# Performance work log

Measured on AMD Instinct MI355X. Metric: run time of the kernel, lower is better.

## Reference

```python
import jax, jax.numpy as jnp
import numpy as np

B, NA, C, NG = 32, 32768, 81, 24
POS_IOU, NEG_IOU, NPR = 0.5, 0.4, 3
VXY, VWH = 0.1, 0.2
NEG_BIG = 1e30


def cxcywh_to_xyxy(b):
    xy, wh = b[..., :2], b[..., 2:]
    return jnp.concatenate([xy - 0.5 * wh, xy + 0.5 * wh], axis=-1)


def box_iou_xyxy(a, g):
    # a: [Na,4], g: [Ng,4] -> [Na,Ng]
    lt = jnp.maximum(a[:, None, :2], g[None, :, :2])
    rb = jnp.minimum(a[:, None, 2:], g[None, :, 2:])
    wh = jnp.clip(rb - lt, 0.0)
    inter = wh[..., 0] * wh[..., 1]
    area_a = (a[:, 2] - a[:, 0]) * (a[:, 3] - a[:, 1])
    area_g = (g[:, 2] - g[:, 0]) * (g[:, 3] - g[:, 1])
    union = area_a[:, None] + area_g[None, :] - inter
    return inter / jnp.maximum(union, 1e-12)


def encode_ssd(gt, anc):
    # gt, anc: [N,4] cxcywh
    txy = (gt[:, :2] - anc[:, :2]) / anc[:, 2:] / VXY
    twh = jnp.log(gt[:, 2:] / anc[:, 2:]) / VWH
    return jnp.concatenate([txy, twh], axis=-1)


def match_one(anchors, gt_b, gt_l):
    # anchors: [Na,4], gt_b: [Ng,4], gt_l: [Ng]
    iou = box_iou_xyxy(cxcywh_to_xyxy(anchors), cxcywh_to_xyxy(gt_b))  # [Na,Ng]
    iou_max = iou.max(axis=1)
    gt_idx = jnp.argmax(iou, axis=1)          # [Na]
    best_anchor = jnp.argmax(iou, axis=0)     # [Ng]
    pos = (iou_max >= POS_IOU).at[best_anchor].set(True)
    ign = (iou_max > NEG_IOU) & ~pos
    cls_t = jnp.where(pos, gt_l[gt_idx].astype(jnp.int32), jnp.where(ign, -1, 0))
    box_t = encode_ssd(gt_b[gt_idx], anchors) * pos[:, None].astype(jnp.float32)
    return cls_t, box_t, pos


def setup_inputs() -> dict:
    key = jax.random.key(0)
    k1, k2, k3, k4, k5, k6, k7 = jax.random.split(key, 7)
    cls_pred = jax.random.normal(k1, (B, NA, C), jnp.float32)
    box_pred = jax.random.normal(k2, (B, NA, 4), jnp.float32) * 0.5
    a_xy = jax.random.uniform(k3, (NA, 2), jnp.float32)
    a_wh = jax.random.uniform(k4, (NA, 2), jnp.float32, minval=0.02, maxval=0.5)
    anchors = jnp.concatenate([a_xy, a_wh], axis=-1)
    g_xy = jax.random.uniform(k5, (B, NG, 2), jnp.float32)
    g_wh = jax.random.uniform(k6, (B, NG, 2), jnp.float32, minval=0.05, maxval=0.4)
    gt_boxes = jnp.concatenate([g_xy, g_wh], axis=-1)
    gt_labels = jax.random.randint(k7, (B, NG), 1, C, jnp.int32)
    return {"cls_pred": cls_pred, "box_pred": box_pred, "anchors": anchors,
            "gt_boxes": gt_boxes, "gt_labels": gt_labels}


def reference(cls_pred, box_pred, anchors, gt_boxes, gt_labels):
    # matching is @torch.no_grad -> constants
    cls_t, box_t, pos = jax.vmap(lambda b, l: match_one(anchors, b, l))(gt_boxes, gt_labels)
    box_t = jax.lax.stop_gradient(box_t)

    logp = jax.nn.log_softmax(cls_pred, axis=-1)
    tgt = jnp.clip(cls_t, 0)
    ce = -jnp.take_along_axis(logp, tgt[..., None], axis=-1)[..., 0]  # [B,Na]

    posf = pos.astype(jnp.float32)
    num_pos = posf.sum(-1)                       # [B]
    pos_ce_sum = (ce * posf).sum(-1)
    neg_mask = cls_t == 0
    neg_count = neg_mask.sum(-1).astype(jnp.float32)

    # descending sort of negative CE (hard-negative mining)
    neg_sorted = -jnp.sort(-jnp.where(neg_mask, ce, -NEG_BIG), axis=-1)  # [B,Na]
    ranks = jnp.arange(NA, dtype=jnp.float32)[None, :]

    num_neg = jnp.minimum(NPR * num_pos, neg_count)
    topk_sum = (neg_sorted * (ranks < num_neg[:, None])).sum(-1)
    cls_pos = jnp.where(num_neg > 0,
                        (pos_ce_sum + topk_sum) / jnp.maximum(num_pos + num_neg, 1.0),
                        pos_ce_sum / jnp.maximum(num_pos, 1.0))

    num_neg0 = jnp.minimum(100.0, neg_count)
    topk0_sum = (neg_sorted * (ranks < num_neg0[:, None])).sum(-1)
    cls_zero = jnp.where(num_neg0 > 0, topk0_sum / jnp.maximum(num_neg0, 1.0), 0.0)

    cls_loss = jnp.where(num_pos > 0, cls_pos, cls_zero)

    d = box_pred - box_t
    ad = jnp.abs(d)
    sl1 = jnp.where(ad < 1.0, 0.5 * d * d, ad - 0.5)
    reg_sum = (sl1 * posf[..., None]).sum((-1, -2))
    reg = jnp.where(num_pos > 0, reg_sum / jnp.maximum(num_pos * 4.0, 1.0), 0.0)

    return cls_loss.mean(), reg.mean(), num_pos.sum() / B
```

## Files before the change

### kernel.cpp

```cpp
#include <hip/hip_runtime.h>
#include <math.h>

#define B_  32
#define NA_ 32768
#define C_  81
#define NG_ 24

typedef const __attribute__((address_space(1))) unsigned int* gas_ptr;
typedef __attribute__((address_space(3))) unsigned int* las_ptr;

__device__ inline float wave_max_f(float v) {
  #pragma unroll
  for (int s = 32; s >= 1; s >>= 1) v = fmaxf(v, __shfl_xor(v, s));
  return v;
}
__device__ inline float wave_sum_f(float v) {
  #pragma unroll
  for (int s = 32; s >= 1; s >>= 1) v += __shfl_xor(v, s);
  return v;
}

__global__ void k_init(unsigned long long* best_packed, int* num_pos_g, int* notneg_g,
                       float* pos_ce_g, float* reg_sum_g) {
  const int t = threadIdx.x + blockIdx.x * blockDim.x;
  if (t < B_ * NG_) best_packed[t] = 0ULL;
  if (t < B_) { num_pos_g[t] = 0; notneg_g[t] = 0; pos_ce_g[t] = 0.f; reg_sum_g[t] = 0.f; }
}

__global__ __launch_bounds__(256) void k_match(
    const float* __restrict__ anchors, const float* __restrict__ gt_boxes,
    float* __restrict__ iou_max_out, int* __restrict__ gt_idx_out,
    unsigned long long* __restrict__ best_packed)
{
  const int b = blockIdx.y;
  const int a = blockIdx.x * 256 + threadIdx.x;
  __shared__ float4 gt_sh[NG_];
  __shared__ float gt_area_sh[NG_];
  __shared__ unsigned long long best_sh[NG_];
  if (threadIdx.x < NG_) {
    const float* g = gt_boxes + ((size_t)b * NG_ + threadIdx.x) * 4;
    float cx = g[0], cy = g[1], w = g[2], h = g[3];
    float x0 = cx - 0.5f * w, y0 = cy - 0.5f * h, x1 = cx + 0.5f * w, y1 = cy + 0.5f * h;
    gt_sh[threadIdx.x] = make_float4(x0, y0, x1, y1);
    gt_area_sh[threadIdx.x] = (x1 - x0) * (y1 - y0);
    best_sh[threadIdx.x] = 0ULL;
  }
  __syncthreads();
  const float4 anc = ((const float4*)anchors)[a];
  const float ax0 = anc.x - 0.5f * anc.z, ay0 = anc.y - 0.5f * anc.w;
  const float ax1 = anc.x + 0.5f * anc.z, ay1 = anc.y + 0.5f * anc.w;
  const float area_a = (ax1 - ax0) * (ay1 - ay0);
  float best_iou = -1.0f; int best_g = 0;
  const int lane = threadIdx.x & 63;
  const int wave_base = a - lane;
  for (int g = 0; g < NG_; ++g) {
    const float4 G = gt_sh[g];
    float lx = fmaxf(ax0, G.x), ly = fmaxf(ay0, G.y);
    float rx = fminf(ax1, G.z), ry = fminf(ay1, G.w);
    float ww = fmaxf(rx - lx, 0.f), hh = fmaxf(ry - ly, 0.f);
    float inter = ww * hh;
    float uni = area_a + gt_area_sh[g] - inter;
    float iou = inter / fmaxf(uni, 1e-12f);
    if (iou > best_iou) { best_iou = iou; best_g = g; }
    const float m = wave_max_f(iou);
    const unsigned long long mk = __ballot(iou == m);
    if (lane == 0) {
      const int amin = wave_base + (__ffsll((long long)mk) - 1);
      const unsigned long long key =
          ((unsigned long long)__float_as_uint(m) << 32) | (unsigned)(~(unsigned)amin);
      atomicMax(&best_sh[g], key);
    }
  }
  const size_t idx = (size_t)b * NA_ + a;
  iou_max_out[idx] = best_iou;
  gt_idx_out[idx]  = best_g;
  __syncthreads();
  if (threadIdx.x < NG_)
    atomicMax(&best_packed[b * NG_ + threadIdx.x], best_sh[threadIdx.x]);
}

#define TPB 128
__global__ __launch_bounds__(128) void k_ce(
    const float* __restrict__ cls_pred, const float* __restrict__ box_pred,
    const float* __restrict__ anchors, const float* __restrict__ gt_boxes,
    const int* __restrict__ gt_labels,
    const float* __restrict__ iou_max_in, const int* __restrict__ gt_idx_in,
    const unsigned long long* __restrict__ best_packed,
    int* __restrict__ neg_bits,
    int* __restrict__ num_pos_g, int* __restrict__ notneg_g,
    float* __restrict__ pos_ce_g, float* __restrict__ reg_sum_g)
{
  __shared__ float tile[TPB * C_];
  __shared__ int best_a_sh[NG_];
  __shared__ int label_sh[NG_];
  __shared__ int np_sh[2], nn_sh[2];
  __shared__ float pce_sh[2], reg_sh[2];
  const int b = blockIdx.y;
  const int tid = threadIdx.x;
  const int wave = tid >> 6, lane = tid & 63;
  const int a0 = blockIdx.x * TPB;
  const int a = a0 + tid;
  const size_t idx = (size_t)b * NA_ + a;

  if (tid < NG_) {
    best_a_sh[tid] = (int)(~(unsigned)(best_packed[b * NG_ + tid]));
    label_sh[tid]  = gt_labels[b * NG_ + tid];
  }

  {
    const unsigned int* gtile =
        (const unsigned int*)(cls_pred + ((size_t)b * NA_ + a0) * C_);
    las_ptr lbase = (las_ptr)tile;
    #pragma unroll
    for (int k = 0; k < 20; ++k) {
      const int chunk = k * TPB + tid;
      const int wbase = k * TPB + wave * 64;
      __builtin_amdgcn_global_load_lds((gas_ptr)(gtile + (size_t)chunk * 4),
                                       lbase + (size_t)wbase * 4, 16, 0, 0);
    }
    if (tid < 32) {
      const int chunk = 20 * TPB + tid;
      __builtin_amdgcn_global_load_lds((gas_ptr)(gtile + (size_t)chunk * 4),
                                       lbase + (size_t)(20 * TPB) * 4, 16, 0, 0);
    }
  }

  const float imax = iou_max_in[idx];
  const int gi = gt_idx_in[idx];
  __syncthreads();

  bool pos = (imax >= 0.5f);
  #pragma unroll
  for (int g = 0; g < NG_; ++g) pos = pos || (best_a_sh[g] == a);
  const bool ign = (imax > 0.4f) && !pos;
  const bool neg = !pos && !ign;
  const int tgt = pos ? label_sh[gi] : 0;

  const float* row = &tile[tid * C_];
  float sum = 0.f;
  #pragma unroll 27
  for (int j = 0; j < C_; ++j) sum += __expf(row[j]);
  float ce = fmaxf(__logf(sum) - row[tgt], 0.f);

  neg_bits[idx] = neg ? __float_as_int(ce) : -1;

  float pce = 0.f, reg = 0.f;
  if (pos) {
    pce = ce;
    const float4 bp = ((const float4*)box_pred)[idx];
    const float4 an = ((const float4*)anchors)[a];
    const float* gt = gt_boxes + ((size_t)b * NG_ + gi) * 4;
    const float tx = (gt[0] - an.x) / an.z / 0.1f;
    const float ty = (gt[1] - an.y) / an.w / 0.1f;
    const float tw = logf(gt[2] / an.z) / 0.2f;
    const float th = logf(gt[3] / an.w) / 0.2f;
    float d, ad;
    d = bp.x - tx; ad = fabsf(d); reg += (ad < 1.f) ? 0.5f * d * d : (ad - 0.5f);
    d = bp.y - ty; ad = fabsf(d); reg += (ad < 1.f) ? 0.5f * d * d : (ad - 0.5f);
    d = bp.z - tw; ad = fabsf(d); reg += (ad < 1.f) ? 0.5f * d * d : (ad - 0.5f);
    d = bp.w - th; ad = fabsf(d); reg += (ad < 1.f) ? 0.5f * d * d : (ad - 0.5f);
  }

  const int np_w = __popcll(__ballot(pos));
  const int nn_w = __popcll(__ballot(pos || ign));
  const float pce_w = wave_sum_f(pce);
  const float reg_w = wave_sum_f(reg);
  if (lane == 0) { np_sh[wave] = np_w; nn_sh[wave] = nn_w; pce_sh[wave] = pce_w; reg_sh[wave] = reg_w; }
  __syncthreads();
  if (tid == 0) {
    const int np = np_sh[0] + np_sh[1];
    const int nn = nn_sh[0] + nn_sh[1];
    const float pc = pce_sh[0] + pce_sh[1];
    const float rg = reg_sh[0] + reg_sh[1];
    if (np) atomicAdd(&num_pos_g[b], np);
    if (nn) atomicAdd(&notneg_g[b], nn);
    if (pc != 0.f) atomicAdd(&pos_ce_g[b], pc);
    if (rg != 0.f) atomicAdd(&reg_sum_g[b], rg);
  }
}

__global__ __launch_bounds__(1024) void k_select(
    const int* __restrict__ neg_bits,
    const int* __restrict__ num_pos_g, const int* __restrict__ notneg_g,
    const float* __restrict__ pos_ce_g, const float* __restrict__ reg_sum_g,
    float* __restrict__ cls_out, float* __restrict__ reg_out)
{
  const int b = blockIdx.x;
  const int t = threadIdx.x;
  const int wave = t >> 6, lane = t & 63;
  int v[32];
  const int* src = neg_bits + (size_t)b * NA_;
  #pragma unroll
  for (int i = 0; i < 32; ++i) v[i] = src[t + (i << 10)];
  const int np = num_pos_g[b];
  const int negc = NA_ - notneg_g[b];
  const int k1 = min(3 * np, negc);
  const int k0 = min(100, negc);
  __shared__ unsigned red_sh[16];
  __shared__ unsigned bc_sh;
  int T1 = 0, T0 = 0;
  for (int bit = 30; bit >= 0; --bit) {
    const int t1 = T1 | (1 << bit);
    const int t0 = T0 | (1 << bit);
    unsigned c = 0;
    #pragma unroll
    for (int i = 0; i < 32; ++i) {
      if (v[i] >= t1) c += (1u << 16);
      if (v[i] >= t0) c += 1u;
    }
    #pragma unroll
    for (int s = 32; s >= 1; s >>= 1) c += __shfl_xor(c, s);
    if (lane == 0) red_sh[wave] = c;
    __syncthreads();
    if (t == 0) {
      unsigned sum = 0;
      for (int w = 0; w < 16; ++w) sum += red_sh[w];
      bc_sh = sum;
    }
    __syncthreads();
    const unsigned sum = bc_sh;
    if ((int)(sum >> 16) >= k1 && k1 > 0) T1 = t1;
    if ((int)(sum & 0xFFFFu) >= k0 && k0 > 0) T0 = t0;
    __syncthreads();
  }
  float s1 = 0.f, s0 = 0.f; unsigned cg = 0;
  #pragma unroll
  for (int i = 0; i < 32; ++i) {
    const int x = v[i];
    if (x > T1) { s1 += __int_as_float(x); cg += (1u << 16); }
    if (x > T0) { s0 += __int_as_float(x); cg += 1u; }
  }
  #pragma unroll
  for (int s = 32; s >= 1; s >>= 1) {
    s1 += __shfl_xor(s1, s); s0 += __shfl_xor(s0, s); cg += __shfl_xor(cg, s);
  }
  __shared__ float f1_sh[16], f0_sh[16]; __shared__ unsigned cg_sh[16];
  if (lane == 0) { f1_sh[wave] = s1; f0_sh[wave] = s0; cg_sh[wave] = cg; }
  __syncthreads();
  if (t == 0) {
    float S1 = 0.f, S0 = 0.f; unsigned CG = 0;
    for (int w = 0; w < 16; ++w) { S1 += f1_sh[w]; S0 += f0_sh[w]; CG += cg_sh[w]; }
    const int cg1 = (int)(CG >> 16), cg0 = (int)(CG & 0xFFFFu);
    const float topk1 = (k1 > 0) ? (S1 + (float)(k1 - cg1) * __int_as_float(T1)) : 0.f;
    const float topk0 = (k0 > 0) ? (S0 + (float)(k0 - cg0) * __int_as_float(T0)) : 0.f;
    const float npf = (float)np;
    const float pce = pos_ce_g[b];
    float cls;
    if (np > 0)
      cls = (k1 > 0) ? (pce + topk1) / fmaxf(npf + (float)k1, 1.f)
                     : pce / fmaxf(npf, 1.f);
    else
      cls = (k0 > 0) ? topk0 / fmaxf((float)k0, 1.f) : 0.f;
    cls_out[b] = cls;
    reg_out[b] = (np > 0) ? reg_sum_g[b] / fmaxf(npf * 4.f, 1.f) : 0.f;
  }
}

__global__ __launch_bounds__(64) void k_final(
    const float* __restrict__ cls_out, const float* __restrict__ reg_out,
    const int* __restrict__ num_pos_g, float* __restrict__ out)
{
  const int t = threadIdx.x;
  float c = (t < B_) ? cls_out[t] : 0.f;
  float r = (t < B_) ? reg_out[t] : 0.f;
  float n = (t < B_) ? (float)num_pos_g[t] : 0.f;
  #pragma unroll
  for (int s = 32; s >= 1; s >>= 1) {
    c += __shfl_xor(c, s); r += __shfl_xor(r, s); n += __shfl_xor(n, s);
  }
  if (t == 0) { out[0] = c / (float)B_; out[1] = r / (float)B_; out[2] = n / (float)B_; }
}

extern "C" void kernel_launch(void* const* d_in, const int* in_sizes, int n_in,
                              void* d_out, int out_size, void* d_ws, size_t ws_size,
                              hipStream_t stream) {
  const float* cls_pred  = (const float*)d_in[0];
  const float* box_pred  = (const float*)d_in[1];
  const float* anchors   = (const float*)d_in[2];
  const float* gt_boxes  = (const float*)d_in[3];
  const int*   gt_labels = (const int*)d_in[4];
  float* out = (float*)d_out;

  char* ws = (char*)d_ws;
  unsigned long long* best_packed = (unsigned long long*)ws;
  int*   num_pos_g = (int*)(ws + 6144);
  int*   notneg_g  = (int*)(ws + 6144 + 128);
  float* pos_ce_g  = (float*)(ws + 6144 + 256);
  float* reg_sum_g = (float*)(ws + 6144 + 384);
  float* cls_out   = (float*)(ws + 6144 + 512);
  float* reg_out   = (float*)(ws + 6144 + 640);
  float* iou_max   = (float*)(ws + 8192);
  int*   gt_idx    = (int*)(ws + 8192 + (size_t)4 * B_ * NA_);
  int*   neg_bits  = (int*)(ws + 8192 + (size_t)8 * B_ * NA_);

  hipLaunchKernelGGL(k_init, dim3(1), dim3(768), 0, stream,
                     best_packed, num_pos_g, notneg_g, pos_ce_g, reg_sum_g);
  hipLaunchKernelGGL(k_match, dim3(NA_ / 256, B_), dim3(256), 0, stream,
                     anchors, gt_boxes, iou_max, gt_idx, best_packed);
  hipLaunchKernelGGL(k_ce, dim3(NA_ / TPB, B_), dim3(TPB), 0, stream,
                     cls_pred, box_pred, anchors, gt_boxes, gt_labels,
                     iou_max, gt_idx, best_packed, neg_bits,
                     num_pos_g, notneg_g, pos_ce_g, reg_sum_g);
  hipLaunchKernelGGL(k_select, dim3(B_), dim3(1024), 0, stream,
                     neg_bits, num_pos_g, notneg_g, pos_ce_g, reg_sum_g, cls_out, reg_out);
  hipLaunchKernelGGL(k_final, dim3(1), dim3(64), 0, stream,
                     cls_out, reg_out, num_pos_g, out);
}
```

Measured before the change: 588.0 us.

## Split per-gt best-anchor search into separate kernel and drop init/final launches

Per-gt best-anchor argmax moves out of the per-anchor match kernel, which did a wave max, ballot and shared atomic every iteration. A new kernel gives each (gt, batch) pair one block that scans all anchors with a packed 64-bit key and reduces with shuffles. The init and final kernels are folded in: counters and the output are zeroed in the new kernel, and the select kernel atomically accumulates the batch means into the output. The select kernel also uses vectorized loads and per-bit shared atomic counters, removing two barriers per radix bit. This trades fewer launches and lighter match work for a redundant full anchor scan per gt (768 blocks) and non-deterministic float atomic ordering in the final output.

```diff
diff --git a/kernel.cpp b/kernel.cpp
--- a/kernel.cpp
+++ b/kernel.cpp
@@ -9,41 +9,31 @@
 typedef const __attribute__((address_space(1))) unsigned int* gas_ptr;
 typedef __attribute__((address_space(3))) unsigned int* las_ptr;
 
-__device__ inline float wave_max_f(float v) {
-  #pragma unroll
-  for (int s = 32; s >= 1; s >>= 1) v = fmaxf(v, __shfl_xor(v, s));
-  return v;
-}
 __device__ inline float wave_sum_f(float v) {
   #pragma unroll
   for (int s = 32; s >= 1; s >>= 1) v += __shfl_xor(v, s);
   return v;
 }
-
-__global__ void k_init(unsigned long long* best_packed, int* num_pos_g, int* notneg_g,
-                       float* pos_ce_g, float* reg_sum_g) {
-  const int t = threadIdx.x + blockIdx.x * blockDim.x;
-  if (t < B_ * NG_) best_packed[t] = 0ULL;
-  if (t < B_) { num_pos_g[t] = 0; notneg_g[t] = 0; pos_ce_g[t] = 0.f; reg_sum_g[t] = 0.f; }
-}
-
-__global__ __launch_bounds__(256) void k_match(
+__device__ inline unsigned long long shflx_u64(unsigned long long v, int s) {
+  int lo = __shfl_xor((int)(unsigned)(v & 0xFFFFFFFFULL), s);
+  int hi = __shfl_xor((int)(unsigned)(v >> 32), s);
+  return ((unsigned long long)(unsigned)hi << 32) | (unsigned)lo;
+}
+
+__global__ __launch_bounds__(256) void k_match_a(
     const float* __restrict__ anchors, const float* __restrict__ gt_boxes,
-    float* __restrict__ iou_max_out, int* __restrict__ gt_idx_out,
-    unsigned long long* __restrict__ best_packed)
+    float* __restrict__ iou_max_out, int* __restrict__ gt_idx_out)
 {
   const int b = blockIdx.y;
   const int a = blockIdx.x * 256 + threadIdx.x;
   __shared__ float4 gt_sh[NG_];
   __shared__ float gt_area_sh[NG_];
-  __shared__ unsigned long long best_sh[NG_];
   if (threadIdx.x < NG_) {
     const float* g = gt_boxes + ((size_t)b * NG_ + threadIdx.x) * 4;
     float cx = g[0], cy = g[1], w = g[2], h = g[3];
     float x0 = cx - 0.5f * w, y0 = cy - 0.5f * h, x1 = cx + 0.5f * w, y1 = cy + 0.5f * h;
     gt_sh[threadIdx.x] = make_float4(x0, y0, x1, y1);
     gt_area_sh[threadIdx.x] = (x1 - x0) * (y1 - y0);
-    best_sh[threadIdx.x] = 0ULL;
   }
   __syncthreads();
   const float4 anc = ((const float4*)anchors)[a];
@@ -51,8 +41,7 @@
   const float ax1 = anc.x + 0.5f * anc.z, ay1 = anc.y + 0.5f * anc.w;
   const float area_a = (ax1 - ax0) * (ay1 - ay0);
   float best_iou = -1.0f; int best_g = 0;
-  const int lane = threadIdx.x & 63;
-  const int wave_base = a - lane;
+  #pragma unroll 4
   for (int g = 0; g < NG_; ++g) {
     const float4 G = gt_sh[g];
     float lx = fmaxf(ax0, G.x), ly = fmaxf(ay0, G.y);
@@ -62,21 +51,57 @@
     float uni = area_a + gt_area_sh[g] - inter;
     float iou = inter / fmaxf(uni, 1e-12f);
     if (iou > best_iou) { best_iou = iou; best_g = g; }
-    const float m = wave_max_f(iou);
-    const unsigned long long mk = __ballot(iou == m);
-    if (lane == 0) {
-      const int amin = wave_base + (__ffsll((long long)mk) - 1);
-      const unsigned long long key =
-          ((unsigned long long)__float_as_uint(m) << 32) | (unsigned)(~(unsigned)amin);
-      atomicMax(&best_sh[g], key);
-    }
   }
   const size_t idx = (size_t)b * NA_ + a;
   iou_max_out[idx] = best_iou;
   gt_idx_out[idx]  = best_g;
-  __syncthreads();
-  if (threadIdx.x < NG_)
-    atomicMax(&best_packed[b * NG_ + threadIdx.x], best_sh[threadIdx.x]);
+}
+
+__global__ __launch_bounds__(256) void k_match_b(
+    const float* __restrict__ anchors, const float* __restrict__ gt_boxes,
+    int* __restrict__ best_anchor,
+    int* num_pos_g, int* notneg_g, float* pos_ce_g, float* reg_sum_g, float* out)
+{
+  const int g = blockIdx.x, b = blockIdx.y;
+  const int tid = threadIdx.x, wave = tid >> 6, lane = tid & 63;
+  if (g == 0 && b == 0) {
+    if (tid < B_) { num_pos_g[tid] = 0; notneg_g[tid] = 0; pos_ce_g[tid] = 0.f; reg_sum_g[tid] = 0.f; }
+    else if (tid < B_ + 3) out[tid - B_] = 0.f;
+  }
+  const float* gp = gt_boxes + ((size_t)b * NG_ + g) * 4;
+  const float gx0 = gp[0] - 0.5f * gp[2], gy0 = gp[1] - 0.5f * gp[3];
+  const float gx1 = gp[0] + 0.5f * gp[2], gy1 = gp[1] + 0.5f * gp[3];
+  const float area_g = (gx1 - gx0) * (gy1 - gy0);
+  unsigned long long key = 0ULL;
+  #pragma unroll 4
+  for (int i = 0; i < NA_ / 256; ++i) {
+    const int a = i * 256 + tid;
+    const float4 anc = ((const float4*)anchors)[a];
+    const float ax0 = anc.x - 0.5f * anc.z, ay0 = anc.y - 0.5f * anc.w;
+    const float ax1 = anc.x + 0.5f * anc.z, ay1 = anc.y + 0.5f * anc.w;
+    float lx = fmaxf(ax0, gx0), ly = fmaxf(ay0, gy0);
+    float rx = fminf(ax1, gx1), ry = fminf(ay1, gy1);
+    float ww = fmaxf(rx - lx, 0.f), hh = fmaxf(ry - ly, 0.f);
+    float inter = ww * hh;
+    float uni = (ax1 - ax0) * (ay1 - ay0) + area_g - inter;
+    float iou = inter / fmaxf(uni, 1e-12f);
+    unsigned long long k2 =
+        ((unsigned long long)__float_as_uint(iou) << 32) | (unsigned)(~(unsigned)a);
+    if (k2 > key) key = k2;
+  }
+  #pragma unroll
+  for (int s = 32; s >= 1; s >>= 1) {
+    unsigned long long o = shflx_u64(key, s);
+    if (o > key) key = o;
+  }
+  __shared__ unsigned long long red[4];
+  if (lane == 0) red[wave] = key;
+  __syncthreads();
+  if (tid == 0) {
+    unsigned long long k = red[0];
+    for (int w = 1; w < 4; ++w) if (red[w] > k) k = red[w];
+    best_anchor[b * NG_ + g] = (int)(~(unsigned)k);
+  }
 }
 
 #define TPB 128
@@ -85,7 +110,7 @@
     const float* __restrict__ anchors, const float* __restrict__ gt_boxes,
     const int* __restrict__ gt_labels,
     const float* __restrict__ iou_max_in, const int* __restrict__ gt_idx_in,
-    const unsigned long long* __restrict__ best_packed,
+    const int* __restrict__ best_anchor,
     int* __restrict__ neg_bits,
     int* __restrict__ num_pos_g, int* __restrict__ notneg_g,
     float* __restrict__ pos_ce_g, float* __restrict__ reg_sum_g)
@@ -103,7 +128,7 @@
   const size_t idx = (size_t)b * NA_ + a;
 
   if (tid < NG_) {
-    best_a_sh[tid] = (int)(~(unsigned)(best_packed[b * NG_ + tid]));
+    best_a_sh[tid] = best_anchor[b * NG_ + tid];
     label_sh[tid]  = gt_labels[b * NG_ + tid];
   }
 
@@ -183,21 +208,24 @@
     const int* __restrict__ neg_bits,
     const int* __restrict__ num_pos_g, const int* __restrict__ notneg_g,
     const float* __restrict__ pos_ce_g, const float* __restrict__ reg_sum_g,
-    float* __restrict__ cls_out, float* __restrict__ reg_out)
+    float* __restrict__ out)
 {
   const int b = blockIdx.x;
   const int t = threadIdx.x;
   const int wave = t >> 6, lane = t & 63;
+  __shared__ unsigned cnt_sh[32];
+  __shared__ float f1_sh[16], f0_sh[16];
+  __shared__ unsigned cg_sh[16];
+  if (t < 32) cnt_sh[t] = 0;
   int v[32];
-  const int* src = neg_bits + (size_t)b * NA_;
-  #pragma unroll
-  for (int i = 0; i < 32; ++i) v[i] = src[t + (i << 10)];
+  const int4* src4 = (const int4*)(neg_bits + (size_t)b * NA_);
+  #pragma unroll
+  for (int i = 0; i < 8; ++i) *(int4*)&v[4 * i] = src4[t + (i << 10)];
   const int np = num_pos_g[b];
   const int negc = NA_ - notneg_g[b];
   const int k1 = min(3 * np, negc);
   const int k0 = min(100, negc);
-  __shared__ unsigned red_sh[16];
-  __shared__ unsigned bc_sh;
+  __syncthreads();
   int T1 = 0, T0 = 0;
   for (int bit = 30; bit >= 0; --bit) {
     const int t1 = T1 | (1 << bit);
@@ -210,18 +238,11 @@
     }
     #pragma unroll
     for (int s = 32; s >= 1; s >>= 1) c += __shfl_xor(c, s);
-    if (lane == 0) red_sh[wave] = c;
+    if (lane == 0) atomicAdd(&cnt_sh[bit], c);
     __syncthreads();
-    if (t == 0) {
-      unsigned sum = 0;
-      for (int w = 0; w < 16; ++w) sum += red_sh[w];
-      bc_sh = sum;
-    }
-    __syncthreads();
-    const unsigned sum = bc_sh;
+    const unsigned sum = cnt_sh[bit];
     if ((int)(sum >> 16) >= k1 && k1 > 0) T1 = t1;
     if ((int)(sum & 0xFFFFu) >= k0 && k0 > 0) T0 = t0;
-    __syncthreads();
   }
   float s1 = 0.f, s0 = 0.f; unsigned cg = 0;
   #pragma unroll
@@ -234,7 +255,6 @@
   for (int s = 32; s >= 1; s >>= 1) {
     s1 += __shfl_xor(s1, s); s0 += __shfl_xor(s0, s); cg += __shfl_xor(cg, s);
   }
-  __shared__ float f1_sh[16], f0_sh[16]; __shared__ unsigned cg_sh[16];
   if (lane == 0) { f1_sh[wave] = s1; f0_sh[wave] = s0; cg_sh[wave] = cg; }
   __syncthreads();
   if (t == 0) {
@@ -251,24 +271,11 @@
                      : pce / fmaxf(npf, 1.f);
     else
       cls = (k0 > 0) ? topk0 / fmaxf((float)k0, 1.f) : 0.f;
-    cls_out[b] = cls;
-    reg_out[b] = (np > 0) ? reg_sum_g[b] / fmaxf(npf * 4.f, 1.f) : 0.f;
-  }
-}
-
-__global__ __launch_bounds__(64) void k_final(
-    const float* __restrict__ cls_out, const float* __restrict__ reg_out,
-    const int* __restrict__ num_pos_g, float* __restrict__ out)
-{
-  const int t = threadIdx.x;
-  float c = (t < B_) ? cls_out[t] : 0.f;
-  float r = (t < B_) ? reg_out[t] : 0.f;
-  float n = (t < B_) ? (float)num_pos_g[t] : 0.f;
-  #pragma unroll
-  for (int s = 32; s >= 1; s >>= 1) {
-    c += __shfl_xor(c, s); r += __shfl_xor(r, s); n += __shfl_xor(n, s);
-  }
-  if (t == 0) { out[0] = c / (float)B_; out[1] = r / (float)B_; out[2] = n / (float)B_; }
+    const float reg = (np > 0) ? reg_sum_g[b] / fmaxf(npf * 4.f, 1.f) : 0.f;
+    atomicAdd(&out[0], cls * (1.0f / B_));
+    atomicAdd(&out[1], reg * (1.0f / B_));
+    atomicAdd(&out[2], npf * (1.0f / B_));
+  }
 }
 
 extern "C" void kernel_launch(void* const* d_in, const int* in_sizes, int n_in,
@@ -282,27 +289,24 @@
   float* out = (float*)d_out;
 
   char* ws = (char*)d_ws;
-  unsigned long long* best_packed = (unsigned long long*)ws;
+  int*   best_anchor = (int*)ws;
   int*   num_pos_g = (int*)(ws + 6144);
   int*   notneg_g  = (int*)(ws + 6144 + 128);
   float* pos_ce_g  = (float*)(ws + 6144 + 256);
   float* reg_sum_g = (float*)(ws + 6144 + 384);
-  float* cls_out   = (float*)(ws + 6144 + 512);
-  float* reg_out   = (float*)(ws + 6144 + 640);
   float* iou_max   = (float*)(ws + 8192);
   int*   gt_idx    = (int*)(ws + 8192 + (size_t)4 * B_ * NA_);
   int*   neg_bits  = (int*)(ws + 8192 + (size_t)8 * B_ * NA_);
 
-  hipLaunchKernelGGL(k_init, dim3(1), dim3(768), 0, stream,
-                     best_packed, num_pos_g, notneg_g, pos_ce_g, reg_sum_g);
-  hipLaunchKernelGGL(k_match, dim3(NA_ / 256, B_), dim3(256), 0, stream,
-                     anchors, gt_boxes, iou_max, gt_idx, best_packed);
+  hipLaunchKernelGGL(k_match_a, dim3(NA_ / 256, B_), dim3(256), 0, stream,
+                     anchors, gt_boxes, iou_max, gt_idx);
+  hipLaunchKernelGGL(k_match_b, dim3(NG_, B_), dim3(256), 0, stream,
+                     anchors, gt_boxes, best_anchor,
+                     num_pos_g, notneg_g, pos_ce_g, reg_sum_g, out);
   hipLaunchKernelGGL(k_ce, dim3(NA_ / TPB, B_), dim3(TPB), 0, stream,
                      cls_pred, box_pred, anchors, gt_boxes, gt_labels,
-                     iou_max, gt_idx, best_packed, neg_bits,
+                     iou_max, gt_idx, best_anchor, neg_bits,
                      num_pos_g, notneg_g, pos_ce_g, reg_sum_g);
   hipLaunchKernelGGL(k_select, dim3(B_), dim3(1024), 0, stream,
-                     neg_bits, num_pos_g, notneg_g, pos_ce_g, reg_sum_g, cls_out, reg_out);
-  hipLaunchKernelGGL(k_final, dim3(1), dim3(64), 0, stream,
-                     cls_out, reg_out, num_pos_g, out);
-}
+                     neg_bits, num_pos_g, notneg_g, pos_ce_g, reg_sum_g, out);
+}
```

New measurement: 584.3 us. About the same (-0.6%).
